# Optimization experiments

Hardware: AMD Instinct MI355X
Metric: run time of the kernel (lower is better)

The kernel has to match this reference:

```python
import jax, jax.numpy as jnp
import numpy as np

NEG = -1e30  # finite stand-in for -inf to keep logsumexp NaN-free


def setup_inputs() -> dict:
    key = jax.random.key(0)
    k1, k2 = jax.random.split(key)
    B, T, C, L = 1024, 256, 128, 48
    # ctc_batch_cost expects softmax probabilities over C classes (blank = C-1)
    y_pred = jax.nn.softmax(jax.random.normal(k1, (B, T, C), dtype=jnp.float32), axis=-1)
    labels = jax.random.randint(k2, (B, L), 0, C - 1, dtype=jnp.int32)  # values in [0, C-2]
    return {"y_pred": y_pred, "labels": labels}


def _lse3(a, b, c):
    m = jnp.maximum(jnp.maximum(a, b), c)
    return m + jnp.log(jnp.exp(a - m) + jnp.exp(b - m) + jnp.exp(c - m))


def reference(y_pred, labels):
    """CTC loss matching keras.backend.ctc_batch_cost (blank = num_classes-1),
    with full input_length=T and label_length=L as in CTCLayer.call.
    Returns per-example loss of shape [B, 1]."""
    eps = 1e-7  # keras.backend.epsilon()
    logp = jnp.log(y_pred + eps)              # [B, T, C]
    B, T, C = y_pred.shape
    L = labels.shape[1]
    S = 2 * L + 1                             # extended label length (blanks interleaved)
    blank = C - 1

    # extended label: blank, l1, blank, l2, ..., lL, blank  -> [B, S]
    ext = jnp.full((B, S), blank, dtype=labels.dtype).at[:, 1::2].set(labels)
    # transition s-2 -> s allowed iff ext[s] != blank and ext[s] != ext[s-2]
    can_skip = jnp.concatenate(
        [jnp.zeros((B, 2), dtype=bool), (ext[:, 2:] != blank) & (ext[:, 2:] != ext[:, :-2])],
        axis=1)                               # [B, S]

    # log-probs gathered at extended-label symbols: [T, B, S]
    lpe = jnp.take_along_axis(jnp.transpose(logp, (1, 0, 2)),
                              jnp.broadcast_to(ext[None], (T, B, S)), axis=2)

    alpha0 = (jnp.full((B, S), NEG, dtype=logp.dtype)
              .at[:, 0].set(lpe[0, :, 0])
              .at[:, 1].set(lpe[0, :, 1]))

    pad1 = jnp.full((B, 1), NEG, dtype=logp.dtype)
    pad2 = jnp.full((B, 2), NEG, dtype=logp.dtype)

    def step(alpha, lp_t):
        a2 = jnp.concatenate([pad1, alpha[:, :-1]], axis=1)
        a3 = jnp.where(can_skip, jnp.concatenate([pad2, alpha[:, :-2]], axis=1), NEG)
        alpha = _lse3(alpha, a2, a3) + lp_t
        return alpha, None

    alphaT, _ = jax.lax.scan(step, alpha0, lpe[1:])
    loss = -jnp.logaddexp(alphaT[:, S - 1], alphaT[:, S - 2])  # end at last blank or last label
    return loss[:, None]                       # [B, 1], matching ctc_batch_cost
```

## Files before the change

kernel.cpp:

```cpp
#include <hip/hip_runtime.h>


#define TT 256
#define CC 128
#define LL 48
#define BS 16
#define NB (TT / BS)

typedef float f32x2 __attribute__((ext_vector_type(2)));

template<int CTRL>
__device__ __forceinline__ float dpp_mv(float x) {
    union { float f; int i; } u, r;
    u.f = x;
    r.i = __builtin_amdgcn_update_dpp(0, u.i, CTRL, 0xF, 0xF, false);
    return r.f;
}
__device__ __forceinline__ float rdlane(float x, int l) {
    union { float f; int i; } u, r;
    u.f = x;
    r.i = __builtin_amdgcn_readlane(u.i, l);
    return r.f;
}

__global__ __launch_bounds__(256) void ctc_fwd_v9(
    const float* __restrict__ y,
    const int* __restrict__ labels,
    float* __restrict__ out)
{
    const int lane = threadIdx.x & 63;
    const int wave = threadIdx.x >> 6;
    const int b = blockIdx.x * 4 + wave;
    const float EPS = 1e-7f;

    int lab = CC - 1;
    if (lane < LL) lab = labels[b * LL + lane];
    const int labprev = __shfl_up(lab, 1);
    const float csf = ((lane > 0) && (lane < LL) && (lab != labprev)) ? 1.0f : 0.0f;
    const int  bidx = (lab >> 1) << 2;
    const bool odd  = (lab & 1);

    const f32x2* p2 = (const f32x2*)(y + (size_t)b * TT * CC) + lane;

    f32x2 A[BS], B[BS], C[BS], D[BS];
    float a0 = (lane == 0) ? 1.0f : 0.0f;
    float a1 = 0.0f;
    int lg = 0;

#define ISSUE(buf, bi_) do {                                              \
    _Pragma("unroll")                                                     \
    for (int _j = 0; _j < BS; ++_j)                                       \
        (buf)[_j] = p2[(size_t)((bi_) * BS + _j) * (CC / 2)];             \
    } while (0)

#define PIN(buf) do {                                                     \
    _Pragma("unroll")                                                     \
    for (int _j = 0; _j < BS; ++_j)                                       \
        asm volatile("" : "+v"((buf)[_j]));   \
    } while (0)

#define STEP2(plv, pbv) do {                                              \
    const float _pp = dpp_mv<0x138>(a1);         \
    const float _a0o = a0;                                                \
    a0 = (_a0o + _pp) * (pbv);                                            \
    a1 = (a1 + _a0o + csf * _pp) * (plv);                                 \
    } while (0)

#define RESCALE do {                                                      \
    float _m = fmaxf(a0, a1);                                             \
    _m = fmaxf(_m, dpp_mv<0x111>(_m));                     \
    _m = fmaxf(_m, dpp_mv<0x112>(_m));                     \
    _m = fmaxf(_m, dpp_mv<0x114>(_m));                     \
    _m = fmaxf(_m, dpp_mv<0x118>(_m));                     \
    _m = fmaxf(_m, dpp_mv<0x142>(_m));                  \
    _m = fmaxf(_m, dpp_mv<0x143>(_m));        \
    const float _mm = rdlane(_m, 63);                                     \
    int _e; (void)frexpf(_mm, &_e);                                       \
    a0 = ldexpf(a0, -_e);                                                 \
    a1 = ldexpf(a1, -_e);                                                 \
    lg += _e;                                                             \
    } while (0)

#define BODY(cons, dst, bi_) do {                                         \
    if ((bi_) + 3 < NB) ISSUE(dst, (bi_) + 3);                            \
    PIN(cons);                                                            \
    float _pl[BS], _pb[BS];                                               \
    _Pragma("unroll")                                                     \
    for (int _k = 0; _k < BS; ++_k) {                                     \
        const int _lo = __builtin_amdgcn_ds_bpermute(bidx, __float_as_int((cons)[_k].x)); \
        const int _hi = __builtin_amdgcn_ds_bpermute(bidx, __float_as_int((cons)[_k].y)); \
        _pl[_k] = __int_as_float(odd ? _hi : _lo) + EPS;                  \
        _pb[_k] = rdlane((cons)[_k].y, 63) + EPS;          \
    }                                                                     \
    _Pragma("unroll")                                                     \
    for (int _k = 0; _k < BS; ++_k) {                                     \
        STEP2(_pl[_k], _pb[_k]);                                          \
        if ((_k & 7) == 7) RESCALE;                                       \
    } } while (0)

    ISSUE(A, 0);
    ISSUE(B, 1);
    ISSUE(C, 2);
    BODY(A, D, 0);  BODY(B, A, 1);  BODY(C, B, 2);  BODY(D, C, 3);
    BODY(A, D, 4);  BODY(B, A, 5);  BODY(C, B, 6);  BODY(D, C, 7);
    BODY(A, D, 8);  BODY(B, A, 9);  BODY(C, B, 10); BODY(D, C, 11);
    BODY(A, D, 12); BODY(B, A, 13); BODY(C, B, 14); BODY(D, C, 15);

    const float v95 = rdlane(a1, 47);
    const float v96 = rdlane(a0, 48);
    if (lane == 0) {
        const float s = fmaxf(v95 + v96, 1e-37f);
        out[b] = -(__logf(s) + (float)lg * 0.69314718056f);
    }

#undef ISSUE
#undef PIN
#undef STEP2
#undef RESCALE
#undef BODY
}

extern "C" void kernel_launch(void* const* d_in, const int* in_sizes, int n_in,
                              void* d_out, int out_size, void* d_ws, size_t ws_size,
                              hipStream_t stream) {
    const float* y = (const float*)d_in[0];
    const int* labels = (const int*)d_in[1];
    float* out = (float*)d_out;
    const int B = in_sizes[0] / (TT * CC);
    ctc_fwd_v9<<<B / 4, 256, 0, stream>>>(y, labels, out);
}
```

Baseline: 28.13 us.

## Split producer/consumer waves with LDS ring buffer for CTC forward

Restructures the kernel so each block handles one batch item with two waves. A producer wave streams chunks of y into a 4-slot LDS ring, and a consumer wave runs the alpha recursion, gathering label and blank probabilities straight from LDS instead of using ds_bpermute and readlane. Producer and consumer synchronize with s_barrier per chunk. This takes the global loads and cross-lane gathers off the serial recursion's critical path, at the cost of barrier overhead, fewer resident batch items per CU and LDS use.

Result: faster. 26.75 us (-4.9%).

```diff
diff --git a/kernel.cpp b/kernel.cpp
--- a/kernel.cpp
+++ b/kernel.cpp
@@ -4,8 +4,8 @@
 #define TT 256
 #define CC 128
 #define LL 48
-#define BS 16
-#define NB (TT / BS)
+#define CH 16
+#define NC (TT / CH)
 
 typedef float f32x2 __attribute__((ext_vector_type(2)));
 
@@ -23,44 +23,60 @@
     return r.f;
 }
 
-__global__ __launch_bounds__(256) void ctc_fwd_v9(
+__global__ __launch_bounds__(128) void ctc_fwd_v10(
     const float* __restrict__ y,
     const int* __restrict__ labels,
     float* __restrict__ out)
 {
+    __shared__ float ring[4][CH][CC];
     const int lane = threadIdx.x & 63;
-    const int wave = threadIdx.x >> 6;
-    const int b = blockIdx.x * 4 + wave;
+    const int w = threadIdx.x >> 6;
+    const int b = blockIdx.x;
     const float EPS = 1e-7f;
 
-    int lab = CC - 1;
-    if (lane < LL) lab = labels[b * LL + lane];
-    const int labprev = __shfl_up(lab, 1);
-    const float csf = ((lane > 0) && (lane < LL) && (lab != labprev)) ? 1.0f : 0.0f;
-    const int  bidx = (lab >> 1) << 2;
-    const bool odd  = (lab & 1);
+    if (w == 1) {
+        const f32x2* p2 = (const f32x2*)(y + (size_t)b * TT * CC) + lane;
+        f32x2 RA[CH], RB[CH], RC[CH];
 
-    const f32x2* p2 = (const f32x2*)(y + (size_t)b * TT * CC) + lane;
-
-    f32x2 A[BS], B[BS], C[BS], D[BS];
-    float a0 = (lane == 0) ? 1.0f : 0.0f;
-    float a1 = 0.0f;
-    int lg = 0;
-
-#define ISSUE(buf, bi_) do {                                              \
+#define LOADP(set, c_) do {                                               \
     _Pragma("unroll")                                                     \
-    for (int _j = 0; _j < BS; ++_j)                                       \
-        (buf)[_j] = p2[(size_t)((bi_) * BS + _j) * (CC / 2)];             \
+    for (int _j = 0; _j < CH; ++_j)                                       \
+        (set)[_j] = p2[(size_t)((c_) * CH + _j) * (CC / 2)];              \
     } while (0)
 
-#define PIN(buf) do {                                                     \
+#define PITER(set, c_) do {                                               \
+    float* _s = &ring[(c_) & 3][0][0];                                    \
     _Pragma("unroll")                                                     \
-    for (int _j = 0; _j < BS; ++_j)                                       \
-        asm volatile("" : "+v"((buf)[_j]));   \
+    for (int _j = 0; _j < CH; ++_j)                                       \
+        *(f32x2*)&_s[_j * CC + 2 * lane] = (set)[_j];   \
+    asm volatile("s_waitcnt lgkmcnt(0)" ::: "memory");                    \
+    __builtin_amdgcn_sched_barrier(0);                                    \
+    __builtin_amdgcn_s_barrier();        \
+    __builtin_amdgcn_sched_barrier(0);                                    \
+    if ((c_) + 3 < NC) LOADP(set, (c_) + 3);                              \
     } while (0)
 
-#define STEP2(plv, pbv) do {                                              \
-    const float _pp = dpp_mv<0x138>(a1);         \
+        LOADP(RA, 0); LOADP(RB, 1); LOADP(RC, 2);
+        PITER(RA, 0);  PITER(RB, 1);  PITER(RC, 2);
+        PITER(RA, 3);  PITER(RB, 4);  PITER(RC, 5);
+        PITER(RA, 6);  PITER(RB, 7);  PITER(RC, 8);
+        PITER(RA, 9);  PITER(RB, 10); PITER(RC, 11);
+        PITER(RA, 12); PITER(RB, 13); PITER(RC, 14);
+        PITER(RA, 15);
+#undef LOADP
+#undef PITER
+    } else {
+        int lab = CC - 1;
+        if (lane < LL) lab = labels[b * LL + lane];
+        const int labprev = __shfl_up(lab, 1);
+        const float csf = ((lane > 0) && (lane < LL) && (lab != labprev)) ? 1.0f : 0.0f;
+
+        float a0 = (lane == 0) ? 1.0f : 0.0f;
+        float a1 = 0.0f;
+        int lg = 0;
+
+#define STEP(plv, pbv) do {                                               \
+    const float _pp = dpp_mv<0x138>(a1);       \
     const float _a0o = a0;                                                \
     a0 = (_a0o + _pp) * (pbv);                                            \
     a1 = (a1 + _a0o + csf * _pp) * (plv);                                 \
@@ -81,43 +97,37 @@
     lg += _e;                                                             \
     } while (0)
 
-#define BODY(cons, dst, bi_) do {                                         \
-    if ((bi_) + 3 < NB) ISSUE(dst, (bi_) + 3);                            \
-    PIN(cons);                                                            \
-    float _pl[BS], _pb[BS];                                               \
+#define CITER(c_) do {                                                    \
+    __builtin_amdgcn_s_barrier();                 \
+    __builtin_amdgcn_sched_barrier(0);                                    \
+    const float* _s = &ring[(c_) & 3][0][0];                              \
+    float _pl[CH], _pb[CH];                                               \
     _Pragma("unroll")                                                     \
-    for (int _k = 0; _k < BS; ++_k) {                                     \
-        const int _lo = __builtin_amdgcn_ds_bpermute(bidx, __float_as_int((cons)[_k].x)); \
-        const int _hi = __builtin_amdgcn_ds_bpermute(bidx, __float_as_int((cons)[_k].y)); \
-        _pl[_k] = __int_as_float(odd ? _hi : _lo) + EPS;                  \
-        _pb[_k] = rdlane((cons)[_k].y, 63) + EPS;          \
+    for (int _r = 0; _r < CH; ++_r) {                                     \
+        _pl[_r] = _s[_r * CC + lab] + EPS;           \
+        _pb[_r] = _s[_r * CC + (CC - 1)] + EPS;       \
     }                                                                     \
     _Pragma("unroll")                                                     \
-    for (int _k = 0; _k < BS; ++_k) {                                     \
-        STEP2(_pl[_k], _pb[_k]);                                          \
-        if ((_k & 7) == 7) RESCALE;                                       \
+    for (int _r = 0; _r < CH; ++_r) {                                     \
+        STEP(_pl[_r], _pb[_r]);                                           \
+        if ((_r & 7) == 7) RESCALE;                                       \
     } } while (0)
 
-    ISSUE(A, 0);
-    ISSUE(B, 1);
-    ISSUE(C, 2);
-    BODY(A, D, 0);  BODY(B, A, 1);  BODY(C, B, 2);  BODY(D, C, 3);
-    BODY(A, D, 4);  BODY(B, A, 5);  BODY(C, B, 6);  BODY(D, C, 7);
-    BODY(A, D, 8);  BODY(B, A, 9);  BODY(C, B, 10); BODY(D, C, 11);
-    BODY(A, D, 12); BODY(B, A, 13); BODY(C, B, 14); BODY(D, C, 15);
+        CITER(0);  CITER(1);  CITER(2);  CITER(3);
+        CITER(4);  CITER(5);  CITER(6);  CITER(7);
+        CITER(8);  CITER(9);  CITER(10); CITER(11);
+        CITER(12); CITER(13); CITER(14); CITER(15);
 
-    const float v95 = rdlane(a1, 47);
-    const float v96 = rdlane(a0, 48);
-    if (lane == 0) {
-        const float s = fmaxf(v95 + v96, 1e-37f);
-        out[b] = -(__logf(s) + (float)lg * 0.69314718056f);
+        const float v95 = rdlane(a1, 47);
+        const float v96 = rdlane(a0, 48);
+        if (lane == 0) {
+            const float s = fmaxf(v95 + v96, 1e-37f);
+            out[b] = -(__logf(s) + (float)lg * 0.69314718056f);
+        }
+#undef STEP
+#undef RESCALE
+#undef CITER
     }
-
-#undef ISSUE
-#undef PIN
-#undef STEP2
-#undef RESCALE
-#undef BODY
 }
 
 extern "C" void kernel_launch(void* const* d_in, const int* in_sizes, int n_in,
@@ -127,5 +137,5 @@
     const int* labels = (const int*)d_in[1];
     float* out = (float*)d_out;
     const int B = in_sizes[0] / (TT * CC);
-    ctc_fwd_v9<<<B / 4, 256, 0, stream>>>(y, labels, out);
+    ctc_fwd_v10<<<B, 128, 0, stream>>>(y, labels, out);
 }
```
